# Kernel tuning notes

Hardware: AMD Instinct MI355X
Metric: run time of the kernel (lower is better)

The kernel has to match this reference:

```python
import jax, jax.numpy as jnp
import numpy as np

N, E, F_IN, HID, HEADS, NT, B = 50000, 400000, 32, 64, 4, 20, 64
IN1 = F_IN + HID  # 96, conv1 input dim after concat with node-type embedding


def _glorot(key, shape):
    fan_in = shape[0]
    return jax.random.normal(key, shape, dtype=jnp.float32) / np.sqrt(fan_in)


def setup_inputs() -> dict:
    key = jax.random.key(0)
    ks = jax.random.split(key, 40)
    inp = {
        "x": jax.random.normal(ks[0], (N, F_IN), dtype=jnp.float32),
        "edge_index": jax.random.randint(ks[1], (2, E), 0, N, dtype=jnp.int32),
        "edge_attr": jax.random.normal(ks[2], (E,), dtype=jnp.float32),
        "batch": jnp.sort(jax.random.randint(ks[3], (N,), 0, B, dtype=jnp.int32)),
        "node_type": jax.random.randint(ks[4], (N,), 0, NT, dtype=jnp.int32),
        # parameters
        "node_emb": jax.random.normal(ks[5], (NT, HID), dtype=jnp.float32) * 0.1,
        "edge_W": _glorot(ks[6], (1, HID)), "edge_b": jnp.zeros((HID,), jnp.float32),
        # GATConv 1 (in=96, out=64, heads=4, edge_dim=64, concat=False)
        "W1": _glorot(ks[7], (IN1, HEADS * HID)),
        "att_src1": jax.random.normal(ks[8], (HEADS, HID), jnp.float32) * 0.1,
        "att_dst1": jax.random.normal(ks[9], (HEADS, HID), jnp.float32) * 0.1,
        "We1": _glorot(ks[10], (HID, HEADS * HID)),
        "att_e1": jax.random.normal(ks[11], (HEADS, HID), jnp.float32) * 0.1,
        "b1": jnp.zeros((HID,), jnp.float32),
        # GATConv 2 (in=64)
        "W2": _glorot(ks[12], (HID, HEADS * HID)),
        "att_src2": jax.random.normal(ks[13], (HEADS, HID), jnp.float32) * 0.1,
        "att_dst2": jax.random.normal(ks[14], (HEADS, HID), jnp.float32) * 0.1,
        "We2": _glorot(ks[15], (HID, HEADS * HID)),
        "att_e2": jax.random.normal(ks[16], (HEADS, HID), jnp.float32) * 0.1,
        "b2": jnp.zeros((HID,), jnp.float32),
        # SAGEConv (mean aggr): out = mean_agg @ Wl + x @ Wr + b
        "sage_Wl": _glorot(ks[17], (HID, HID)), "sage_Wr": _glorot(ks[18], (HID, HID)),
        "sage_b": jnp.zeros((HID,), jnp.float32),
        "lin1_W": _glorot(ks[19], (HID, HID)), "lin1_b": jnp.zeros((HID,), jnp.float32),
        "lin2_W": _glorot(ks[20], (HID, HID)), "lin2_b": jnp.zeros((HID,), jnp.float32),
        "tel_W": _glorot(ks[21], (HID, 1)), "tel_b": jnp.zeros((1,), jnp.float32),
        "comp_W": _glorot(ks[22], (HID, 1)), "comp_b": jnp.zeros((1,), jnp.float32),
        "pch_W": _glorot(ks[23], (HID, 1)), "pch_b": jnp.zeros((1,), jnp.float32),
    }
    return inp


def _gat(x, src, dst, edge_h, W, att_s, att_d, We, att_e, b):
    n = x.shape[0]
    h = (x @ W).reshape(n, HEADS, HID)                       # [N,H,C]
    a_s = (h * att_s).sum(-1)                                # [N,H]
    a_d = (h * att_d).sum(-1)
    e = (edge_h @ We).reshape(-1, HEADS, HID)                # [E,H,C]
    a_e = (e * att_e).sum(-1)                                # [E,H]
    alpha = jax.nn.leaky_relu(a_s[src] + a_d[dst] + a_e, 0.2)
    m = jax.ops.segment_max(alpha, dst, num_segments=n)
    m = jnp.where(jnp.isfinite(m), m, 0.0)
    ex = jnp.exp(alpha - m[dst])
    den = jax.ops.segment_sum(ex, dst, num_segments=n)
    alpha = ex / (den[dst] + 1e-16)                          # segment softmax per dst
    out = jax.ops.segment_sum(h[src] * alpha[..., None], dst, num_segments=n)
    return out.mean(axis=1) + b                              # concat=False -> head mean


def reference(x, edge_index, edge_attr, batch, node_type, node_emb, edge_W, edge_b,
              W1, att_src1, att_dst1, We1, att_e1, b1,
              W2, att_src2, att_dst2, We2, att_e2, b2,
              sage_Wl, sage_Wr, sage_b, lin1_W, lin1_b, lin2_W, lin2_b,
              tel_W, tel_b, comp_W, comp_b, pch_W, pch_b):
    src, dst = edge_index[0], edge_index[1]
    edge_h = edge_attr[:, None] @ edge_W + edge_b            # [E,HID]
    h = jnp.concatenate([x, node_emb[node_type]], axis=-1)   # [N,96]
    h = jax.nn.elu(_gat(h, src, dst, edge_h, W1, att_src1, att_dst1, We1, att_e1, b1))
    h = jax.nn.elu(_gat(h, src, dst, edge_h, W2, att_src2, att_dst2, We2, att_e2, b2))
    # SAGEConv with mean aggregation
    deg = jax.ops.segment_sum(jnp.ones((src.shape[0],), h.dtype), dst, num_segments=N)
    agg = jax.ops.segment_sum(h[src], dst, num_segments=N) / jnp.maximum(deg, 1.0)[:, None]
    h = jax.nn.elu(agg @ sage_Wl + h @ sage_Wr + sage_b)
    # global mean pool over graphs
    cnt = jax.ops.segment_sum(jnp.ones((N,), h.dtype), batch, num_segments=B)
    g = jax.ops.segment_sum(h, batch, num_segments=B) / jnp.maximum(cnt, 1.0)[:, None]
    g = jax.nn.elu(g @ lin1_W + lin1_b)                      # dropout is identity in eval
    g = g @ lin2_W + lin2_b
    return (g @ tel_W + tel_b, g @ comp_W + comp_b, g @ pch_W + pch_b)
```

## Files before the change

kernel.cpp:

```cpp
#include <hip/hip_runtime.h>
#include <hip/hip_bf16.h>


#define NN 50000
#define NE 400000
#define FIN 32
#define NBATCH 64

typedef __hip_bfloat16 bf16;
typedef short bf16x8 __attribute__((ext_vector_type(8)));
typedef float f32x4 __attribute__((ext_vector_type(4)));

__device__ __forceinline__ float b2f(bf16 v) { return __bfloat162float(v); }
__device__ __forceinline__ float lrelu(float x) { return x > 0.f ? x : 0.2f * x; }
__device__ __forceinline__ float eluf(float x) { return x > 0.f ? x : (expf(x) - 1.f); }

__device__ __forceinline__ float4 f4fma(float s, float4 w, float4 c) {
  c.x = fmaf(s, w.x, c.x); c.y = fmaf(s, w.y, c.y);
  c.z = fmaf(s, w.z, c.z); c.w = fmaf(s, w.w, c.w);
  return c;
}

__device__ __forceinline__ float4 upk4(uint2 u) {
  float4 f;
  f.x = __uint_as_float(u.x << 16);
  f.y = __uint_as_float(u.x & 0xffff0000u);
  f.z = __uint_as_float(u.y << 16);
  f.w = __uint_as_float(u.y & 0xffff0000u);
  return f;
}

__device__ __forceinline__ unsigned short bfbits(float f) {
  bf16 b = __float2bfloat16(f);
  unsigned short u;
  __builtin_memcpy(&u, &b, 2);
  return u;
}
__device__ __forceinline__ float hi_f(unsigned short u) {
  return __uint_as_float((unsigned int)u << 16);
}

__global__ __launch_bounds__(256) void k_prep(
    const float* __restrict__ W1, const float* __restrict__ W2,
    const float* __restrict__ We1, const float* __restrict__ atte1,
    const float* __restrict__ We2, const float* __restrict__ atte2,
    const float* __restrict__ edgeW, const float* __restrict__ edgeB,
    unsigned short* __restrict__ B1h, unsigned short* __restrict__ B1l,
    unsigned short* __restrict__ B2h, unsigned short* __restrict__ B2l,
    float* __restrict__ pq) {
  if (blockIdx.x == 96) {
    int t = threadIdx.x, h = t >> 6, c = t & 63;
    float sW1 = 0.f, sB1 = 0.f, sW2 = 0.f, sB2 = 0.f;
    for (int j = 0; j < 64; ++j) {
      float w = edgeW[j], b = edgeB[j];
      float we1 = We1[j * 256 + h * 64 + c];
      float we2 = We2[j * 256 + h * 64 + c];
      sW1 += w * we1; sB1 += b * we1;
      sW2 += w * we2; sB2 += b * we2;
    }
    float a1 = atte1[h * 64 + c], a2 = atte2[h * 64 + c];
    float p1 = sW1 * a1, q1 = sB1 * a1, p2 = sW2 * a2, q2 = sB2 * a2;
    for (int o = 32; o; o >>= 1) {
      p1 += __shfl_xor(p1, o); q1 += __shfl_xor(q1, o);
      p2 += __shfl_xor(p2, o); q2 += __shfl_xor(q2, o);
    }
    if (c == 0) { pq[h] = p1; pq[4 + h] = q1; pq[8 + h] = p2; pq[12 + h] = q2; }
    return;
  }
  int t = blockIdx.x * 256 + threadIdx.x;
  if (t < 256 * 96) {
    int n = t / 96, k = t - n * 96;
    float v = W1[k * 256 + n];
    unsigned short h = bfbits(v);
    B1h[t] = h; B1l[t] = bfbits(v - hi_f(h));
  }
  if (t < 256 * 64) {
    int n = t >> 6, k = t & 63;
    float v = W2[k * 256 + n];
    unsigned short h = bfbits(v);
    B2h[t] = h; B2l[t] = bfbits(v - hi_f(h));
  }
}

__global__ void k_hist(const int* __restrict__ dst, int* __restrict__ cnt) {
  int e = blockIdx.x * 256 + threadIdx.x;
  if (e < NE) atomicAdd(&cnt[dst[e]], 1);
}

__global__ __launch_bounds__(1024) void k_scan(const int* __restrict__ cnt,
                                               int* __restrict__ off) {
  __shared__ int wsum[16];
  __shared__ int carry;
  int t = threadIdx.x, lane = t & 63, w = t >> 6;
  if (t == 0) { carry = 0; off[0] = 0; }
  __syncthreads();
  for (int base = 0; base < NN; base += 1024) {
    int idx = base + t;
    int v = (idx < NN) ? cnt[idx] : 0;
    int s = v;
    for (int o = 1; o < 64; o <<= 1) { int u = __shfl_up(s, o); if (lane >= o) s += u; }
    if (lane == 63) wsum[w] = s;
    __syncthreads();
    if (t < 16) {
      int ws = wsum[t];
      for (int o = 1; o < 16; o <<= 1) { int u = __shfl_up(ws, o); if (t >= o) ws += u; }
      wsum[t] = ws;
    }
    __syncthreads();
    int add = carry + (w ? wsum[w - 1] : 0);
    if (idx < NN) off[idx + 1] = add + s;
    __syncthreads();
    if (t == 0) carry += wsum[15];
    __syncthreads();
  }
}

__global__ void k_scatter(const int* __restrict__ src, const int* __restrict__ dst,
                          const float* __restrict__ ea, const int* __restrict__ off,
                          int* __restrict__ cnt, int* __restrict__ csr_src,
                          float* __restrict__ csr_ea) {
  int e = blockIdx.x * 256 + threadIdx.x;
  if (e >= NE) return;
  int d = dst[e];
  int r = atomicSub(&cnt[d], 1);
  int slot = off[d] + r - 1;
  csr_src[slot] = src[e];
  csr_ea[slot] = ea[e];
}

__global__ __launch_bounds__(256) void k_splitA(
    const float* __restrict__ x, const int* __restrict__ ntype,
    const float* __restrict__ emb, unsigned short* __restrict__ Ah,
    unsigned short* __restrict__ Al) {
  const int total = NN * 96;
  for (int i = blockIdx.x * 256 + threadIdx.x; i < total; i += gridDim.x * 256) {
    int n = i / 96, k = i - n * 96;
    float v = (k < FIN) ? x[n * FIN + k] : emb[ntype[n] * 64 + (k - FIN)];
    unsigned short h = bfbits(v);
    Ah[i] = h;
    Al[i] = bfbits(v - hi_f(h));
  }
}

template <int K>
__global__ __launch_bounds__(256) void k_mm_mfma(
    const unsigned short* __restrict__ Ah, const unsigned short* __restrict__ Al,
    const unsigned short* __restrict__ Bh, const unsigned short* __restrict__ Bl,
    const float* __restrict__ atts, const float* __restrict__ attd,
    bf16* __restrict__ hmat, float* __restrict__ as_, float* __restrict__ ad_) {
  int m0 = blockIdx.x * 64;
  int w = threadIdx.x >> 6;
  int lane = threadIdx.x & 63;
  int lr = lane & 15;
  int lc = lane >> 4;
  float attsv[4], attdv[4];
  #pragma unroll
  for (int nt = 0; nt < 4; ++nt) {
    attsv[nt] = atts[w * 64 + nt * 16 + lr];
    attdv[nt] = attd[w * 64 + nt * 16 + lr];
  }
  f32x4 acc[4][4] = {};
  #pragma unroll
  for (int ks = 0; ks < K; ks += 32) {
    int koff = ks + lc * 8;
    bf16x8 ah[4], al[4], bh[4], bl[4];
    #pragma unroll
    for (int mt = 0; mt < 4; ++mt) {
      int m = m0 + mt * 16 + lr;
      if (m > NN - 1) m = NN - 1;
      ah[mt] = *reinterpret_cast<const bf16x8*>(&Ah[(size_t)m * K + koff]);
      al[mt] = *reinterpret_cast<const bf16x8*>(&Al[(size_t)m * K + koff]);
    }
    #pragma unroll
    for (int nt = 0; nt < 4; ++nt) {
      int n = w * 64 + nt * 16 + lr;
      bh[nt] = *reinterpret_cast<const bf16x8*>(&Bh[(size_t)n * K + koff]);
      bl[nt] = *reinterpret_cast<const bf16x8*>(&Bl[(size_t)n * K + koff]);
    }
    #pragma unroll
    for (int mt = 0; mt < 4; ++mt) {
      #pragma unroll
      for (int nt = 0; nt < 4; ++nt) {
        acc[mt][nt] = __builtin_amdgcn_mfma_f32_16x16x32_bf16(ah[mt], bh[nt], acc[mt][nt], 0, 0, 0);
        acc[mt][nt] = __builtin_amdgcn_mfma_f32_16x16x32_bf16(al[mt], bh[nt], acc[mt][nt], 0, 0, 0);
        acc[mt][nt] = __builtin_amdgcn_mfma_f32_16x16x32_bf16(ah[mt], bl[nt], acc[mt][nt], 0, 0, 0);
      }
    }
  }
  #pragma unroll
  for (int mt = 0; mt < 4; ++mt) {
    #pragma unroll
    for (int reg = 0; reg < 4; ++reg) {
      int row = m0 + mt * 16 + lc * 4 + reg;
      float sS = 0.f, sD = 0.f;
      #pragma unroll
      for (int nt = 0; nt < 4; ++nt) {
        float v = acc[mt][nt][reg];
        sS += v * attsv[nt];
        sD += v * attdv[nt];
      }
      for (int o = 1; o < 16; o <<= 1) {
        sS += __shfl_xor(sS, o);
        sD += __shfl_xor(sD, o);
      }
      if (row < NN) {
        #pragma unroll
        for (int nt = 0; nt < 4; ++nt)
          hmat[(size_t)row * 256 + w * 64 + nt * 16 + lr] =
              __float2bfloat16(acc[mt][nt][reg]);
        if (lr == 0) { as_[row * 4 + w] = sS; ad_[row * 4 + w] = sD; }
      }
    }
  }
}

__global__ __launch_bounds__(256) void k_gat(
    const int* __restrict__ off, const int* __restrict__ csr_src,
    const float* __restrict__ csr_ea, const float* __restrict__ as_,
    const float* __restrict__ ad_, const float* __restrict__ pq, int pqo,
    const bf16* __restrict__ hmat, const float* __restrict__ bias,
    float* __restrict__ outf, unsigned short* __restrict__ oph,
    unsigned short* __restrict__ opl) {
  __shared__ float wlds[4][256];
  int wv = threadIdx.x >> 6;
  int wid = (blockIdx.x << 2) + wv;
  int lane = threadIdx.x & 63;
  if (wid >= NN) return;
  int beg = off[wid], end = off[wid + 1];
  int deg = end - beg;
  int hsel = lane >> 4;
  float4 D = reinterpret_cast<const float4*>(ad_)[wid];
  float p0 = pq[pqo + 0], p1 = pq[pqo + 1], p2 = pq[pqo + 2], p3 = pq[pqo + 3];
  float q0 = pq[pqo + 4], q1 = pq[pqo + 5], q2 = pq[pqo + 6], q3 = pq[pqo + 7];
  float4 acc = {0.f, 0.f, 0.f, 0.f};

  if (deg <= 64) {
    bool valid = lane < deg;
    float lx = -INFINITY, ly = -INFINITY, lz = -INFINITY, lw = -INFINITY;
    if (valid) {
      int s = csr_src[beg + lane];
      float ea = csr_ea[beg + lane];
      float4 A = reinterpret_cast<const float4*>(as_)[s];
      lx = lrelu(A.x + D.x + ea * p0 + q0);
      ly = lrelu(A.y + D.y + ea * p1 + q1);
      lz = lrelu(A.z + D.z + ea * p2 + q2);
      lw = lrelu(A.w + D.w + ea * p3 + q3);
    }
    float m0 = lx, m1 = ly, m2 = lz, m3 = lw;
    for (int o = 32; o; o >>= 1) {
      m0 = fmaxf(m0, __shfl_xor(m0, o));
      m1 = fmaxf(m1, __shfl_xor(m1, o));
      m2 = fmaxf(m2, __shfl_xor(m2, o));
      m3 = fmaxf(m3, __shfl_xor(m3, o));
    }
    float w0 = valid ? __expf(lx - m0) : 0.f;
    float w1 = valid ? __expf(ly - m1) : 0.f;
    float w2 = valid ? __expf(lz - m2) : 0.f;
    float w3 = valid ? __expf(lw - m3) : 0.f;
    float s0 = w0, s1 = w1, s2 = w2, s3 = w3;
    for (int o = 32; o; o >>= 1) {
      s0 += __shfl_xor(s0, o); s1 += __shfl_xor(s1, o);
      s2 += __shfl_xor(s2, o); s3 += __shfl_xor(s3, o);
    }
    float4 wv4;
    wv4.x = w0 / (s0 + 1e-16f);
    wv4.y = w1 / (s1 + 1e-16f);
    wv4.z = w2 / (s2 + 1e-16f);
    wv4.w = w3 / (s3 + 1e-16f);
    reinterpret_cast<float4*>(&wlds[wv][0])[lane] = wv4;
    const float* wp = &wlds[wv][0];
    int j = 0;
    for (; j + 8 <= deg; j += 8) {
      int sA = csr_src[beg + j + 0];
      int sB = csr_src[beg + j + 1];
      int sC = csr_src[beg + j + 2];
      int sD = csr_src[beg + j + 3];
      int sE = csr_src[beg + j + 4];
      int sF = csr_src[beg + j + 5];
      int sG = csr_src[beg + j + 6];
      int sH = csr_src[beg + j + 7];
      float wA = wp[4 * (j + 0) + hsel];
      float wB = wp[4 * (j + 1) + hsel];
      float wC = wp[4 * (j + 2) + hsel];
      float wD = wp[4 * (j + 3) + hsel];
      float wE = wp[4 * (j + 4) + hsel];
      float wF = wp[4 * (j + 5) + hsel];
      float wG = wp[4 * (j + 6) + hsel];
      float wH = wp[4 * (j + 7) + hsel];
      uint2 uA = *reinterpret_cast<const uint2*>(&hmat[(size_t)sA * 256 + 4 * lane]);
      uint2 uB = *reinterpret_cast<const uint2*>(&hmat[(size_t)sB * 256 + 4 * lane]);
      uint2 uC = *reinterpret_cast<const uint2*>(&hmat[(size_t)sC * 256 + 4 * lane]);
      uint2 uD = *reinterpret_cast<const uint2*>(&hmat[(size_t)sD * 256 + 4 * lane]);
      uint2 uE = *reinterpret_cast<const uint2*>(&hmat[(size_t)sE * 256 + 4 * lane]);
      uint2 uF = *reinterpret_cast<const uint2*>(&hmat[(size_t)sF * 256 + 4 * lane]);
      uint2 uG = *reinterpret_cast<const uint2*>(&hmat[(size_t)sG * 256 + 4 * lane]);
      uint2 uH = *reinterpret_cast<const uint2*>(&hmat[(size_t)sH * 256 + 4 * lane]);
      acc = f4fma(wA, upk4(uA), acc);
      acc = f4fma(wB, upk4(uB), acc);
      acc = f4fma(wC, upk4(uC), acc);
      acc = f4fma(wD, upk4(uD), acc);
      acc = f4fma(wE, upk4(uE), acc);
      acc = f4fma(wF, upk4(uF), acc);
      acc = f4fma(wG, upk4(uG), acc);
      acc = f4fma(wH, upk4(uH), acc);
    }
    for (; j + 4 <= deg; j += 4) {
      int sA = csr_src[beg + j + 0];
      int sB = csr_src[beg + j + 1];
      int sC = csr_src[beg + j + 2];
      int sD = csr_src[beg + j + 3];
      float wA = wp[4 * (j + 0) + hsel];
      float wB = wp[4 * (j + 1) + hsel];
      float wC = wp[4 * (j + 2) + hsel];
      float wD = wp[4 * (j + 3) + hsel];
      uint2 uA = *reinterpret_cast<const uint2*>(&hmat[(size_t)sA * 256 + 4 * lane]);
      uint2 uB = *reinterpret_cast<const uint2*>(&hmat[(size_t)sB * 256 + 4 * lane]);
      uint2 uC = *reinterpret_cast<const uint2*>(&hmat[(size_t)sC * 256 + 4 * lane]);
      uint2 uD = *reinterpret_cast<const uint2*>(&hmat[(size_t)sD * 256 + 4 * lane]);
      acc = f4fma(wA, upk4(uA), acc);
      acc = f4fma(wB, upk4(uB), acc);
      acc = f4fma(wC, upk4(uC), acc);
      acc = f4fma(wD, upk4(uD), acc);
    }
    for (; j < deg; ++j) {
      int s = csr_src[beg + j];
      float w = wp[4 * j + hsel];
      uint2 u = *reinterpret_cast<const uint2*>(&hmat[(size_t)s * 256 + 4 * lane]);
      acc = f4fma(w, upk4(u), acc);
    }
  } else {
    float m0 = -INFINITY, m1 = -INFINITY, m2 = -INFINITY, m3 = -INFINITY;
    float s0 = 0.f, s1 = 0.f, s2 = 0.f, s3 = 0.f;
    for (int e = beg + lane; e < end; e += 64) {
      int s = csr_src[e];
      float ea = csr_ea[e];
      float4 A = reinterpret_cast<const float4*>(as_)[s];
      float lx = lrelu(A.x + D.x + ea * p0 + q0);
      float ly = lrelu(A.y + D.y + ea * p1 + q1);
      float lz = lrelu(A.z + D.z + ea * p2 + q2);
      float lw = lrelu(A.w + D.w + ea * p3 + q3);
      float nm;
      nm = fmaxf(m0, lx); s0 = s0 * __expf(m0 - nm) + __expf(lx - nm); m0 = nm;
      nm = fmaxf(m1, ly); s1 = s1 * __expf(m1 - nm) + __expf(ly - nm); m1 = nm;
      nm = fmaxf(m2, lz); s2 = s2 * __expf(m2 - nm) + __expf(lz - nm); m2 = nm;
      nm = fmaxf(m3, lw); s3 = s3 * __expf(m3 - nm) + __expf(lw - nm); m3 = nm;
    }
    for (int o = 32; o; o >>= 1) {
      float om, os, nm;
      om = __shfl_xor(m0, o); os = __shfl_xor(s0, o); nm = fmaxf(m0, om);
      s0 = s0 * __expf(fmaxf(m0 - nm, -80.f)) + os * __expf(fmaxf(om - nm, -80.f)); m0 = nm;
      om = __shfl_xor(m1, o); os = __shfl_xor(s1, o); nm = fmaxf(m1, om);
      s1 = s1 * __expf(fmaxf(m1 - nm, -80.f)) + os * __expf(fmaxf(om - nm, -80.f)); m1 = nm;
      om = __shfl_xor(m2, o); os = __shfl_xor(s2, o); nm = fmaxf(m2, om);
      s2 = s2 * __expf(fmaxf(m2 - nm, -80.f)) + os * __expf(fmaxf(om - nm, -80.f)); m2 = nm;
      om = __shfl_xor(m3, o); os = __shfl_xor(s3, o); nm = fmaxf(m3, om);
      s3 = s3 * __expf(fmaxf(m3 - nm, -80.f)) + os * __expf(fmaxf(om - nm, -80.f)); m3 = nm;
    }
    float i0 = 1.f / (s0 + 1e-16f), i1 = 1.f / (s1 + 1e-16f);
    float i2 = 1.f / (s2 + 1e-16f), i3 = 1.f / (s3 + 1e-16f);
    float Dh = hsel == 0 ? D.x : hsel == 1 ? D.y : hsel == 2 ? D.z : D.w;
    float ph = hsel == 0 ? p0 : hsel == 1 ? p1 : hsel == 2 ? p2 : p3;
    float qh = hsel == 0 ? q0 : hsel == 1 ? q1 : hsel == 2 ? q2 : q3;
    float mh = hsel == 0 ? m0 : hsel == 1 ? m1 : hsel == 2 ? m2 : m3;
    float ih = hsel == 0 ? i0 : hsel == 1 ? i1 : hsel == 2 ? i2 : i3;
    for (int j = beg; j < end; ++j) {
      int s = csr_src[j];
      float ea = csr_ea[j];
      float4 A = reinterpret_cast<const float4*>(as_)[s];
      float Ah = hsel == 0 ? A.x : hsel == 1 ? A.y : hsel == 2 ? A.z : A.w;
      float l = lrelu(Ah + Dh + ea * ph + qh);
      float w = __expf(l - mh) * ih;
      uint2 u = *reinterpret_cast<const uint2*>(&hmat[(size_t)s * 256 + 4 * lane]);
      acc = f4fma(w, upk4(u), acc);
    }
  }
  acc.x += __shfl_xor(acc.x, 16); acc.y += __shfl_xor(acc.y, 16);
  acc.z += __shfl_xor(acc.z, 16); acc.w += __shfl_xor(acc.w, 16);
  acc.x += __shfl_xor(acc.x, 32); acc.y += __shfl_xor(acc.y, 32);
  acc.z += __shfl_xor(acc.z, 32); acc.w += __shfl_xor(acc.w, 32);
  if (lane < 16) {
    float4 bv = reinterpret_cast<const float4*>(bias)[lane];
    float4 r;
    r.x = eluf(0.25f * acc.x + bv.x);
    r.y = eluf(0.25f * acc.y + bv.y);
    r.z = eluf(0.25f * acc.z + bv.z);
    r.w = eluf(0.25f * acc.w + bv.w);
    if (outf) reinterpret_cast<float4*>(&outf[(size_t)wid * 64])[lane] = r;
    if (oph) {
      ushort4 h4, l4;
      h4.x = bfbits(r.x); l4.x = bfbits(r.x - hi_f(h4.x));
      h4.y = bfbits(r.y); l4.y = bfbits(r.y - hi_f(h4.y));
      h4.z = bfbits(r.z); l4.z = bfbits(r.z - hi_f(h4.z));
      h4.w = bfbits(r.w); l4.w = bfbits(r.w - hi_f(h4.w));
      *reinterpret_cast<ushort4*>(&oph[(size_t)wid * 64 + lane * 4]) = h4;
      *reinterpret_cast<ushort4*>(&opl[(size_t)wid * 64 + lane * 4]) = l4;
    }
  }
}

__global__ __launch_bounds__(256) void k_agg(
    const int* __restrict__ off, const int* __restrict__ csr_src,
    const float* __restrict__ h3, float* __restrict__ agg) {
  int wid = (blockIdx.x << 2) + (threadIdx.x >> 6);
  int lane = threadIdx.x & 63;
  if (wid >= NN) return;
  int beg = off[wid], end = off[wid + 1];
  float acc = 0.f;
  int e = beg;
  for (; e + 8 <= end; e += 8) {
    int s0 = csr_src[e + 0], s1 = csr_src[e + 1];
    int s2 = csr_src[e + 2], s3 = csr_src[e + 3];
    int s4 = csr_src[e + 4], s5 = csr_src[e + 5];
    int s6 = csr_src[e + 6], s7 = csr_src[e + 7];
    float v0 = h3[(size_t)s0 * 64 + lane];
    float v1 = h3[(size_t)s1 * 64 + lane];
    float v2 = h3[(size_t)s2 * 64 + lane];
    float v3 = h3[(size_t)s3 * 64 + lane];
    float v4 = h3[(size_t)s4 * 64 + lane];
    float v5 = h3[(size_t)s5 * 64 + lane];
    float v6 = h3[(size_t)s6 * 64 + lane];
    float v7 = h3[(size_t)s7 * 64 + lane];
    acc += ((v0 + v1) + (v2 + v3)) + ((v4 + v5) + (v6 + v7));
  }
  for (; e + 4 <= end; e += 4) {
    int s0 = csr_src[e + 0], s1 = csr_src[e + 1];
    int s2 = csr_src[e + 2], s3 = csr_src[e + 3];
    float v0 = h3[(size_t)s0 * 64 + lane];
    float v1 = h3[(size_t)s1 * 64 + lane];
    float v2 = h3[(size_t)s2 * 64 + lane];
    float v3 = h3[(size_t)s3 * 64 + lane];
    acc += (v0 + v1) + (v2 + v3);
  }
  for (; e < end; ++e) acc += h3[(size_t)csr_src[e] * 64 + lane];
  agg[(size_t)wid * 64 + lane] = acc / fmaxf((float)(end - beg), 1.f);
}

__global__ __launch_bounds__(256) void k_sage_mm(
    const float* __restrict__ agg, const float* __restrict__ h3,
    const float* __restrict__ Wl, const float* __restrict__ Wr,
    const float* __restrict__ bias, float* __restrict__ out) {
  __shared__ float WlS[4096];
  __shared__ float WrS[4096];
  __shared__ float Ag[2048];
  __shared__ float Hr[2048];
  int t = threadIdx.x;
  for (int i = t; i < 4096; i += 256) { WlS[i] = Wl[i]; WrS[i] = Wr[i]; }
  int ct = t & 15, rg = t >> 4;
  float4 bv = reinterpret_cast<const float4*>(bias)[ct];
  for (int r0 = blockIdx.x * 32; r0 < NN; r0 += gridDim.x * 32) {
    for (int i = t; i < 2048; i += 256) {
      int n = r0 + (i >> 6);
      float va = 0.f, vh = 0.f;
      if (n < NN) {
        va = agg[(size_t)n * 64 + (i & 63)];
        vh = h3[(size_t)n * 64 + (i & 63)];
      }
      Ag[i] = va; Hr[i] = vh;
    }
    __syncthreads();
    float4 c0 = {0.f, 0.f, 0.f, 0.f}, c1 = c0;
    const float* a0 = &Ag[(rg * 2 + 0) * 64];
    const float* a1 = &Ag[(rg * 2 + 1) * 64];
    const float* h0 = &Hr[(rg * 2 + 0) * 64];
    const float* h1 = &Hr[(rg * 2 + 1) * 64];
    #pragma unroll 4
    for (int k = 0; k < 64; k += 4) {
      float4 wl0 = *reinterpret_cast<const float4*>(&WlS[(k + 0) * 64 + ct * 4]);
      float4 wl1 = *reinterpret_cast<const float4*>(&WlS[(k + 1) * 64 + ct * 4]);
      float4 wl2 = *reinterpret_cast<const float4*>(&WlS[(k + 2) * 64 + ct * 4]);
      float4 wl3 = *reinterpret_cast<const float4*>(&WlS[(k + 3) * 64 + ct * 4]);
      float4 wr0 = *reinterpret_cast<const float4*>(&WrS[(k + 0) * 64 + ct * 4]);
      float4 wr1 = *reinterpret_cast<const float4*>(&WrS[(k + 1) * 64 + ct * 4]);
      float4 wr2 = *reinterpret_cast<const float4*>(&WrS[(k + 2) * 64 + ct * 4]);
      float4 wr3 = *reinterpret_cast<const float4*>(&WrS[(k + 3) * 64 + ct * 4]);
      float4 aa0 = *reinterpret_cast<const float4*>(&a0[k]);
      float4 aa1 = *reinterpret_cast<const float4*>(&a1[k]);
      float4 hh0 = *reinterpret_cast<const float4*>(&h0[k]);
      float4 hh1 = *reinterpret_cast<const float4*>(&h1[k]);
      c0 = f4fma(aa0.x, wl0, c0); c0 = f4fma(aa0.y, wl1, c0);
      c0 = f4fma(aa0.z, wl2, c0); c0 = f4fma(aa0.w, wl3, c0);
      c0 = f4fma(hh0.x, wr0, c0); c0 = f4fma(hh0.y, wr1, c0);
      c0 = f4fma(hh0.z, wr2, c0); c0 = f4fma(hh0.w, wr3, c0);
      c1 = f4fma(aa1.x, wl0, c1); c1 = f4fma(aa1.y, wl1, c1);
      c1 = f4fma(aa1.z, wl2, c1); c1 = f4fma(aa1.w, wl3, c1);
      c1 = f4fma(hh1.x, wr0, c1); c1 = f4fma(hh1.y, wr1, c1);
      c1 = f4fma(hh1.z, wr2, c1); c1 = f4fma(hh1.w, wr3, c1);
    }
    int n0 = r0 + rg * 2;
    if (n0 + 0 < NN) {
      float4 r;
      r.x = eluf(c0.x + bv.x); r.y = eluf(c0.y + bv.y);
      r.z = eluf(c0.z + bv.z); r.w = eluf(c0.w + bv.w);
      *reinterpret_cast<float4*>(&out[(size_t)(n0 + 0) * 64 + ct * 4]) = r;
    }
    if (n0 + 1 < NN) {
      float4 r;
      r.x = eluf(c1.x + bv.x); r.y = eluf(c1.y + bv.y);
      r.z = eluf(c1.z + bv.z); r.w = eluf(c1.w + bv.w);
      *reinterpret_cast<float4*>(&out[(size_t)(n0 + 1) * 64 + ct * 4]) = r;
    }
    __syncthreads();
  }
}

__global__ __launch_bounds__(256) void k_pool2(const float* __restrict__ hs,
                                               const int* __restrict__ batch,
                                               float* __restrict__ g) {
  int cid = (blockIdx.x << 2) + (threadIdx.x >> 6);
  int lane = threadIdx.x & 63;
  int n0 = cid * 32;
  if (n0 >= NN) return;
  int n1 = n0 + 32 < NN ? n0 + 32 : NN;
  int cur = batch[n0];
  float acc = 0.f;
  for (int n = n0; n < n1; ++n) {
    int b = batch[n];
    if (b != cur) {
      atomicAdd(&g[cur * 64 + lane], acc);
      acc = 0.f;
      cur = b;
    }
    acc += hs[(size_t)n * 64 + lane];
  }
  atomicAdd(&g[cur * 64 + lane], acc);
}

__device__ __forceinline__ int lowerb(const int* __restrict__ a, int n, int key) {
  int lo = 0, hi = n;
  while (lo < hi) { int mid = (lo + hi) >> 1; if (a[mid] < key) lo = mid + 1; else hi = mid; }
  return lo;
}

__global__ __launch_bounds__(256) void k_head(
    const float* __restrict__ g, const int* __restrict__ batch,
    const float* __restrict__ l1W, const float* __restrict__ l1b,
    const float* __restrict__ l2W, const float* __restrict__ l2b,
    const float* __restrict__ telW, const float* __restrict__ telb,
    const float* __restrict__ compW, const float* __restrict__ compb,
    const float* __restrict__ pchW, const float* __restrict__ pchb,
    float* __restrict__ out) {
  __shared__ float gS[4096];
  __shared__ float WS[4096];
  __shared__ float hS[4096];
  __shared__ float invc[64];
  int t = threadIdx.x;
  if (t < 64) {
    int lo = lowerb(batch, NN, t), hi = lowerb(batch, NN, t + 1);
    invc[t] = 1.f / fmaxf((float)(hi - lo), 1.f);
  }
  for (int i = t; i < 4096; i += 256) WS[i] = l1W[i];
  __syncthreads();
  for (int i = t; i < 4096; i += 256) gS[i] = g[i] * invc[i >> 6];
  __syncthreads();
  for (int i = t; i < 4096; i += 256) {
    int r = i >> 6, j = i & 63;
    float s = 0.f;
    for (int k = 0; k < 64; ++k) s += gS[r * 64 + k] * WS[k * 64 + j];
    hS[i] = eluf(s + l1b[j]);
  }
  __syncthreads();
  for (int i = t; i < 4096; i += 256) WS[i] = l2W[i];
  __syncthreads();
  for (int i = t; i < 4096; i += 256) {
    int r = i >> 6, j = i & 63;
    float s = 0.f;
    for (int k = 0; k < 64; ++k) s += hS[r * 64 + k] * WS[k * 64 + j];
    gS[i] = s + l2b[j];
  }
  __syncthreads();
  if (t < 192) {
    int head = t >> 6, r = t & 63;
    const float* Wv = head == 0 ? telW : (head == 1 ? compW : pchW);
    float bb = head == 0 ? telb[0] : (head == 1 ? compb[0] : pchb[0]);
    float s = 0.f;
    for (int k = 0; k < 64; ++k) s += gS[r * 64 + k] * Wv[k];
    out[t] = s + bb;
  }
}

extern "C" void kernel_launch(void* const* d_in, const int* in_sizes, int n_in,
                              void* d_out, int out_size, void* d_ws, size_t ws_size,
                              hipStream_t stream) {
  const float* x     = (const float*)d_in[0];
  const int*   eidx  = (const int*)d_in[1];
  const float* eattr = (const float*)d_in[2];
  const int*   batch = (const int*)d_in[3];
  const int*   ntype = (const int*)d_in[4];
  const float* nemb  = (const float*)d_in[5];
  const float* edgeW = (const float*)d_in[6];
  const float* edgeB = (const float*)d_in[7];
  const float* W1    = (const float*)d_in[8];
  const float* atts1 = (const float*)d_in[9];
  const float* attd1 = (const float*)d_in[10];
  const float* We1   = (const float*)d_in[11];
  const float* atte1 = (const float*)d_in[12];
  const float* b1    = (const float*)d_in[13];
  const float* W2    = (const float*)d_in[14];
  const float* atts2 = (const float*)d_in[15];
  const float* attd2 = (const float*)d_in[16];
  const float* We2   = (const float*)d_in[17];
  const float* atte2 = (const float*)d_in[18];
  const float* b2    = (const float*)d_in[19];
  const float* sageWl = (const float*)d_in[20];
  const float* sageWr = (const float*)d_in[21];
  const float* sageB  = (const float*)d_in[22];
  const float* l1W = (const float*)d_in[23];
  const float* l1b = (const float*)d_in[24];
  const float* l2W = (const float*)d_in[25];
  const float* l2b = (const float*)d_in[26];
  const float* telW  = (const float*)d_in[27];
  const float* telb  = (const float*)d_in[28];
  const float* compW = (const float*)d_in[29];
  const float* compb = (const float*)d_in[30];
  const float* pchW  = (const float*)d_in[31];
  const float* pchb  = (const float*)d_in[32];

  char* wp = (char*)d_ws;
  auto alloc = [&](size_t bytes) -> char* {
    char* p = wp;
    wp += (bytes + 255) & ~(size_t)255;
    return p;
  };
  float*  pq      = (float*)alloc(16 * 4);
  int*    cnt     = (int*)alloc((size_t)NN * 4);
  int*    off     = (int*)alloc(((size_t)NN + 1) * 4);
  int*    csr_src = (int*)alloc((size_t)NE * 4);
  float*  csr_ea  = (float*)alloc((size_t)NE * 4);
  float*  as_     = (float*)alloc((size_t)NN * 16);
  float*  ad_     = (float*)alloc((size_t)NN * 16);
  bf16*   hmat    = (bf16*)alloc((size_t)NN * 256 * 2);
  float*  nodeB   = (float*)alloc((size_t)NN * 64 * 4);
  float*  aggbuf  = (float*)alloc((size_t)NN * 64 * 4);
  unsigned short* B1h = (unsigned short*)alloc(256 * 96 * 2);
  unsigned short* B1l = (unsigned short*)alloc(256 * 96 * 2);
  unsigned short* B2h = (unsigned short*)alloc(256 * 64 * 2);
  unsigned short* B2l = (unsigned short*)alloc(256 * 64 * 2);
  char* R = alloc((size_t)NN * 96 * 2 * 2);
  unsigned short* A1h = (unsigned short*)R;
  unsigned short* A1l = A1h + (size_t)NN * 96;
  unsigned short* A2h = (unsigned short*)R;
  unsigned short* A2l = A2h + (size_t)NN * 64;
  float* sageout = (float*)R;
  float* gbuf = (float*)alloc(64 * 64 * 4);

  const int* srcI = eidx;
  const int* dstI = eidx + NE;

  hipMemsetAsync(cnt, 0, (size_t)NN * 4, stream);
  hipMemsetAsync(gbuf, 0, 64 * 64 * 4, stream);
  k_prep<<<97, 256, 0, stream>>>(W1, W2, We1, atte1, We2, atte2, edgeW, edgeB,
                                 B1h, B1l, B2h, B2l, pq);
  k_hist<<<(NE + 255) / 256, 256, 0, stream>>>(dstI, cnt);
  k_scan<<<1, 1024, 0, stream>>>(cnt, off);
  k_scatter<<<(NE + 255) / 256, 256, 0, stream>>>(srcI, dstI, eattr, off, cnt,
                                                  csr_src, csr_ea);
  k_splitA<<<2048, 256, 0, stream>>>(x, ntype, nemb, A1h, A1l);
  k_mm_mfma<96><<<(NN + 63) / 64, 256, 0, stream>>>(
      A1h, A1l, B1h, B1l, atts1, attd1, hmat, as_, ad_);
  k_gat<<<NN / 4, 256, 0, stream>>>(off, csr_src, csr_ea, as_, ad_, pq, 0,
                                    hmat, b1, nullptr, A2h, A2l);
  k_mm_mfma<64><<<(NN + 63) / 64, 256, 0, stream>>>(
      A2h, A2l, B2h, B2l, atts2, attd2, hmat, as_, ad_);
  k_gat<<<NN / 4, 256, 0, stream>>>(off, csr_src, csr_ea, as_, ad_, pq, 8,
                                    hmat, b2, nodeB, nullptr, nullptr);
  k_agg<<<NN / 4, 256, 0, stream>>>(off, csr_src, nodeB, aggbuf);
  k_sage_mm<<<1024, 256, 0, stream>>>(aggbuf, nodeB, sageWl, sageWr, sageB,
                                      sageout);
  k_pool2<<<((NN + 31) / 32 + 3) / 4, 256, 0, stream>>>(sageout, batch, gbuf);
  k_head<<<1, 256, 0, stream>>>(gbuf, batch, l1W, l1b, l2W, l2b, telW, telb,
                                compW, compb, pchW, pchb, (float*)d_out);
}
```

Measured before the change: 452.2 us.

## Fuse SAGE aggregation, matmul and mean-pool; merge prep, splitA and memsets

The SAGE neighbor-mean aggregation, the dense SAGE matmul and the global pooling atomics now run in a single kernel. Aggregated rows and outputs stay in shared memory, so the agg and sageout buffers are never written to or read back from global memory. The weight split, input split and buffer zeroing are also merged into one prep kernel, replacing two memsets and two launches. The trade-off is more shared memory and per-block weight loading across about 1563 blocks, where the old matmul kernel used 1024 persistent blocks.

Measured after the change: 496.0 us. +9.7%, slower.

```diff
diff --git a/kernel.cpp b/kernel.cpp
--- a/kernel.cpp
+++ b/kernel.cpp
@@ -40,23 +40,28 @@
   return __uint_as_float((unsigned int)u << 16);
 }
 
-__global__ __launch_bounds__(256) void k_prep(
-    const float* __restrict__ W1, const float* __restrict__ W2,
-    const float* __restrict__ We1, const float* __restrict__ atte1,
-    const float* __restrict__ We2, const float* __restrict__ atte2,
-    const float* __restrict__ edgeW, const float* __restrict__ edgeB,
-    unsigned short* __restrict__ B1h, unsigned short* __restrict__ B1l,
-    unsigned short* __restrict__ B2h, unsigned short* __restrict__ B2l,
-    float* __restrict__ pq) {
-  if (blockIdx.x == 96) {
-    int t = threadIdx.x, h = t >> 6, c = t & 63;
+__global__ __launch_bounds__(256) void k_prep0(
+    const float* __restrict__ x, const int* __restrict__ ntype,
+    const float* __restrict__ emb, unsigned short* __restrict__ A1h,
+    unsigned short* __restrict__ A1l, const float* __restrict__ W1,
+    const float* __restrict__ W2, const float* __restrict__ We1,
+    const float* __restrict__ atte1, const float* __restrict__ We2,
+    const float* __restrict__ atte2, const float* __restrict__ edgeW,
+    const float* __restrict__ edgeB, unsigned short* __restrict__ B1h,
+    unsigned short* __restrict__ B1l, unsigned short* __restrict__ B2h,
+    unsigned short* __restrict__ B2l, float* __restrict__ pq,
+    int* __restrict__ cnt, float* __restrict__ gbuf) {
+  int b = blockIdx.x;
+  int tid = threadIdx.x;
+  if (b == 0) {
+    int h = tid >> 6, c = tid & 63;
     float sW1 = 0.f, sB1 = 0.f, sW2 = 0.f, sB2 = 0.f;
     for (int j = 0; j < 64; ++j) {
-      float w = edgeW[j], b = edgeB[j];
+      float w = edgeW[j], bb = edgeB[j];
       float we1 = We1[j * 256 + h * 64 + c];
       float we2 = We2[j * 256 + h * 64 + c];
-      sW1 += w * we1; sB1 += b * we1;
-      sW2 += w * we2; sB2 += b * we2;
+      sW1 += w * we1; sB1 += bb * we1;
+      sW2 += w * we2; sB2 += bb * we2;
     }
     float a1 = atte1[h * 64 + c], a2 = atte2[h * 64 + c];
     float p1 = sW1 * a1, q1 = sB1 * a1, p2 = sW2 * a2, q2 = sB2 * a2;
@@ -67,19 +72,35 @@
     if (c == 0) { pq[h] = p1; pq[4 + h] = q1; pq[8 + h] = p2; pq[12 + h] = q2; }
     return;
   }
-  int t = blockIdx.x * 256 + threadIdx.x;
-  if (t < 256 * 96) {
-    int n = t / 96, k = t - n * 96;
-    float v = W1[k * 256 + n];
+  if (b <= 96) {
+    int t = (b - 1) * 256 + tid;
+    if (t < 256 * 96) {
+      int n = t / 96, k = t - n * 96;
+      float v = W1[k * 256 + n];
+      unsigned short h = bfbits(v);
+      B1h[t] = h; B1l[t] = bfbits(v - hi_f(h));
+    }
+    if (t < 256 * 64) {
+      int n = t >> 6, k = t & 63;
+      float v = W2[k * 256 + n];
+      unsigned short h = bfbits(v);
+      B2h[t] = h; B2l[t] = bfbits(v - hi_f(h));
+    }
+    return;
+  }
+  int nb = gridDim.x - 97;
+  int base = (b - 97) * 256 + tid;
+  int stride = nb * 256;
+  const int total = NN * 96;
+  for (int i = base; i < total; i += stride) {
+    int n = i / 96, k = i - n * 96;
+    float v = (k < FIN) ? x[n * FIN + k] : emb[ntype[n] * 64 + (k - FIN)];
     unsigned short h = bfbits(v);
-    B1h[t] = h; B1l[t] = bfbits(v - hi_f(h));
-  }
-  if (t < 256 * 64) {
-    int n = t >> 6, k = t & 63;
-    float v = W2[k * 256 + n];
-    unsigned short h = bfbits(v);
-    B2h[t] = h; B2l[t] = bfbits(v - hi_f(h));
-  }
+    A1h[i] = h;
+    A1l[i] = bfbits(v - hi_f(h));
+  }
+  for (int i = base; i < NN; i += stride) cnt[i] = 0;
+  for (int i = base; i < 64 * 64; i += stride) gbuf[i] = 0.f;
 }
 
 __global__ void k_hist(const int* __restrict__ dst, int* __restrict__ cnt) {
@@ -126,20 +147,6 @@
   int slot = off[d] + r - 1;
   csr_src[slot] = src[e];
   csr_ea[slot] = ea[e];
-}
-
-__global__ __launch_bounds__(256) void k_splitA(
-    const float* __restrict__ x, const int* __restrict__ ntype,
-    const float* __restrict__ emb, unsigned short* __restrict__ Ah,
-    unsigned short* __restrict__ Al) {
-  const int total = NN * 96;
-  for (int i = blockIdx.x * 256 + threadIdx.x; i < total; i += gridDim.x * 256) {
-    int n = i / 96, k = i - n * 96;
-    float v = (k < FIN) ? x[n * FIN + k] : emb[ntype[n] * 64 + (k - FIN)];
-    unsigned short h = bfbits(v);
-    Ah[i] = h;
-    Al[i] = bfbits(v - hi_f(h));
-  }
 }
 
 template <int K>
@@ -398,131 +405,106 @@
   }
 }
 
-__global__ __launch_bounds__(256) void k_agg(
+__global__ __launch_bounds__(256) void k_sage_f(
     const int* __restrict__ off, const int* __restrict__ csr_src,
-    const float* __restrict__ h3, float* __restrict__ agg) {
-  int wid = (blockIdx.x << 2) + (threadIdx.x >> 6);
-  int lane = threadIdx.x & 63;
-  if (wid >= NN) return;
-  int beg = off[wid], end = off[wid + 1];
-  float acc = 0.f;
-  int e = beg;
-  for (; e + 8 <= end; e += 8) {
-    int s0 = csr_src[e + 0], s1 = csr_src[e + 1];
-    int s2 = csr_src[e + 2], s3 = csr_src[e + 3];
-    int s4 = csr_src[e + 4], s5 = csr_src[e + 5];
-    int s6 = csr_src[e + 6], s7 = csr_src[e + 7];
-    float v0 = h3[(size_t)s0 * 64 + lane];
-    float v1 = h3[(size_t)s1 * 64 + lane];
-    float v2 = h3[(size_t)s2 * 64 + lane];
-    float v3 = h3[(size_t)s3 * 64 + lane];
-    float v4 = h3[(size_t)s4 * 64 + lane];
-    float v5 = h3[(size_t)s5 * 64 + lane];
-    float v6 = h3[(size_t)s6 * 64 + lane];
-    float v7 = h3[(size_t)s7 * 64 + lane];
-    acc += ((v0 + v1) + (v2 + v3)) + ((v4 + v5) + (v6 + v7));
-  }
-  for (; e + 4 <= end; e += 4) {
-    int s0 = csr_src[e + 0], s1 = csr_src[e + 1];
-    int s2 = csr_src[e + 2], s3 = csr_src[e + 3];
-    float v0 = h3[(size_t)s0 * 64 + lane];
-    float v1 = h3[(size_t)s1 * 64 + lane];
-    float v2 = h3[(size_t)s2 * 64 + lane];
-    float v3 = h3[(size_t)s3 * 64 + lane];
-    acc += (v0 + v1) + (v2 + v3);
-  }
-  for (; e < end; ++e) acc += h3[(size_t)csr_src[e] * 64 + lane];
-  agg[(size_t)wid * 64 + lane] = acc / fmaxf((float)(end - beg), 1.f);
-}
-
-__global__ __launch_bounds__(256) void k_sage_mm(
-    const float* __restrict__ agg, const float* __restrict__ h3,
-    const float* __restrict__ Wl, const float* __restrict__ Wr,
-    const float* __restrict__ bias, float* __restrict__ out) {
+    const float* __restrict__ h3, const float* __restrict__ Wl,
+    const float* __restrict__ Wr, const float* __restrict__ bias,
+    const int* __restrict__ batch, float* __restrict__ g) {
   __shared__ float WlS[4096];
   __shared__ float WrS[4096];
   __shared__ float Ag[2048];
   __shared__ float Hr[2048];
-  int t = threadIdx.x;
+  __shared__ float Out[2048];
+  __shared__ int bS[32];
+  int t = threadIdx.x, lane = t & 63, w = t >> 6;
   for (int i = t; i < 4096; i += 256) { WlS[i] = Wl[i]; WrS[i] = Wr[i]; }
+  int r0 = blockIdx.x * 32;
+  for (int k = 0; k < 8; ++k) {
+    int rl = w * 8 + k;
+    int n = r0 + rl;
+    float aggv = 0.f, hv = 0.f;
+    int bb = -1;
+    if (n < NN) {
+      int beg = off[n], end = off[n + 1];
+      float acc = 0.f;
+      int e = beg;
+      for (; e + 8 <= end; e += 8) {
+        int s0 = csr_src[e + 0], s1 = csr_src[e + 1];
+        int s2 = csr_src[e + 2], s3 = csr_src[e + 3];
+        int s4 = csr_src[e + 4], s5 = csr_src[e + 5];
+        int s6 = csr_src[e + 6], s7 = csr_src[e + 7];
+        float v0 = h3[(size_t)s0 * 64 + lane];
+        float v1 = h3[(size_t)s1 * 64 + lane];
+        float v2 = h3[(size_t)s2 * 64 + lane];
+        float v3 = h3[(size_t)s3 * 64 + lane];
+        float v4 = h3[(size_t)s4 * 64 + lane];
+        float v5 = h3[(size_t)s5 * 64 + lane];
+        float v6 = h3[(size_t)s6 * 64 + lane];
+        float v7 = h3[(size_t)s7 * 64 + lane];
+        acc += ((v0 + v1) + (v2 + v3)) + ((v4 + v5) + (v6 + v7));
+      }
+      for (; e < end; ++e) acc += h3[(size_t)csr_src[e] * 64 + lane];
+      aggv = acc / fmaxf((float)(end - beg), 1.f);
+      hv = h3[(size_t)n * 64 + lane];
+      bb = batch[n];
+    }
+    Ag[rl * 64 + lane] = aggv;
+    Hr[rl * 64 + lane] = hv;
+    if (lane == 0) bS[rl] = bb;
+  }
+  __syncthreads();
   int ct = t & 15, rg = t >> 4;
   float4 bv = reinterpret_cast<const float4*>(bias)[ct];
-  for (int r0 = blockIdx.x * 32; r0 < NN; r0 += gridDim.x * 32) {
-    for (int i = t; i < 2048; i += 256) {
-      int n = r0 + (i >> 6);
-      float va = 0.f, vh = 0.f;
-      if (n < NN) {
-        va = agg[(size_t)n * 64 + (i & 63)];
-        vh = h3[(size_t)n * 64 + (i & 63)];
-      }
-      Ag[i] = va; Hr[i] = vh;
-    }
-    __syncthreads();
-    float4 c0 = {0.f, 0.f, 0.f, 0.f}, c1 = c0;
-    const float* a0 = &Ag[(rg * 2 + 0) * 64];
-    const float* a1 = &Ag[(rg * 2 + 1) * 64];
-    const float* h0 = &Hr[(rg * 2 + 0) * 64];
-    const float* h1 = &Hr[(rg * 2 + 1) * 64];
-    #pragma unroll 4
-    for (int k = 0; k < 64; k += 4) {
-      float4 wl0 = *reinterpret_cast<const float4*>(&WlS[(k + 0) * 64 + ct * 4]);
-      float4 wl1 = *reinterpret_cast<const float4*>(&WlS[(k + 1) * 64 + ct * 4]);
-      float4 wl2 = *reinterpret_cast<const float4*>(&WlS[(k + 2) * 64 + ct * 4]);
-      float4 wl3 = *reinterpret_cast<const float4*>(&WlS[(k + 3) * 64 + ct * 4]);
-      float4 wr0 = *reinterpret_cast<const float4*>(&WrS[(k + 0) * 64 + ct * 4]);
-      float4 wr1 = *reinterpret_cast<const float4*>(&WrS[(k + 1) * 64 + ct * 4]);
-      float4 wr2 = *reinterpret_cast<const float4*>(&WrS[(k + 2) * 64 + ct * 4]);
-      float4 wr3 = *reinterpret_cast<const float4*>(&WrS[(k + 3) * 64 + ct * 4]);
-      float4 aa0 = *reinterpret_cast<const float4*>(&a0[k]);
-      float4 aa1 = *reinterpret_cast<const float4*>(&a1[k]);
-      float4 hh0 = *reinterpret_cast<const float4*>(&h0[k]);
-      float4 hh1 = *reinterpret_cast<const float4*>(&h1[k]);
-      c0 = f4fma(aa0.x, wl0, c0); c0 = f4fma(aa0.y, wl1, c0);
-      c0 = f4fma(aa0.z, wl2, c0); c0 = f4fma(aa0.w, wl3, c0);
-      c0 = f4fma(hh0.x, wr0, c0); c0 = f4fma(hh0.y, wr1, c0);
-      c0 = f4fma(hh0.z, wr2, c0); c0 = f4fma(hh0.w, wr3, c0);
-      c1 = f4fma(aa1.x, wl0, c1); c1 = f4fma(aa1.y, wl1, c1);
-      c1 = f4fma(aa1.z, wl2, c1); c1 = f4fma(aa1.w, wl3, c1);
-      c1 = f4fma(hh1.x, wr0, c1); c1 = f4fma(hh1.y, wr1, c1);
-      c1 = f4fma(hh1.z, wr2, c1); c1 = f4fma(hh1.w, wr3, c1);
-    }
-    int n0 = r0 + rg * 2;
-    if (n0 + 0 < NN) {
-      float4 r;
-      r.x = eluf(c0.x + bv.x); r.y = eluf(c0.y + bv.y);
-      r.z = eluf(c0.z + bv.z); r.w = eluf(c0.w + bv.w);
-      *reinterpret_cast<float4*>(&out[(size_t)(n0 + 0) * 64 + ct * 4]) = r;
-    }
-    if (n0 + 1 < NN) {
-      float4 r;
-      r.x = eluf(c1.x + bv.x); r.y = eluf(c1.y + bv.y);
-      r.z = eluf(c1.z + bv.z); r.w = eluf(c1.w + bv.w);
-      *reinterpret_cast<float4*>(&out[(size_t)(n0 + 1) * 64 + ct * 4]) = r;
-    }
-    __syncthreads();
-  }
-}
-
-__global__ __launch_bounds__(256) void k_pool2(const float* __restrict__ hs,
-                                               const int* __restrict__ batch,
-                                               float* __restrict__ g) {
-  int cid = (blockIdx.x << 2) + (threadIdx.x >> 6);
-  int lane = threadIdx.x & 63;
-  int n0 = cid * 32;
-  if (n0 >= NN) return;
-  int n1 = n0 + 32 < NN ? n0 + 32 : NN;
-  int cur = batch[n0];
+  float4 c0 = {0.f, 0.f, 0.f, 0.f}, c1 = c0;
+  const float* a0 = &Ag[(rg * 2 + 0) * 64];
+  const float* a1 = &Ag[(rg * 2 + 1) * 64];
+  const float* h0 = &Hr[(rg * 2 + 0) * 64];
+  const float* h1 = &Hr[(rg * 2 + 1) * 64];
+  #pragma unroll 4
+  for (int k = 0; k < 64; k += 4) {
+    float4 wl0 = *reinterpret_cast<const float4*>(&WlS[(k + 0) * 64 + ct * 4]);
+    float4 wl1 = *reinterpret_cast<const float4*>(&WlS[(k + 1) * 64 + ct * 4]);
+    float4 wl2 = *reinterpret_cast<const float4*>(&WlS[(k + 2) * 64 + ct * 4]);
+    float4 wl3 = *reinterpret_cast<const float4*>(&WlS[(k + 3) * 64 + ct * 4]);
+    float4 wr0 = *reinterpret_cast<const float4*>(&WrS[(k + 0) * 64 + ct * 4]);
+    float4 wr1 = *reinterpret_cast<const float4*>(&WrS[(k + 1) * 64 + ct * 4]);
+    float4 wr2 = *reinterpret_cast<const float4*>(&WrS[(k + 2) * 64 + ct * 4]);
+    float4 wr3 = *reinterpret_cast<const float4*>(&WrS[(k + 3) * 64 + ct * 4]);
+    float4 aa0 = *reinterpret_cast<const float4*>(&a0[k]);
+    float4 aa1 = *reinterpret_cast<const float4*>(&a1[k]);
+    float4 hh0 = *reinterpret_cast<const float4*>(&h0[k]);
+    float4 hh1 = *reinterpret_cast<const float4*>(&h1[k]);
+    c0 = f4fma(aa0.x, wl0, c0); c0 = f4fma(aa0.y, wl1, c0);
+    c0 = f4fma(aa0.z, wl2, c0); c0 = f4fma(aa0.w, wl3, c0);
+    c0 = f4fma(hh0.x, wr0, c0); c0 = f4fma(hh0.y, wr1, c0);
+    c0 = f4fma(hh0.z, wr2, c0); c0 = f4fma(hh0.w, wr3, c0);
+    c1 = f4fma(aa1.x, wl0, c1); c1 = f4fma(aa1.y, wl1, c1);
+    c1 = f4fma(aa1.z, wl2, c1); c1 = f4fma(aa1.w, wl3, c1);
+    c1 = f4fma(hh1.x, wr0, c1); c1 = f4fma(hh1.y, wr1, c1);
+    c1 = f4fma(hh1.z, wr2, c1); c1 = f4fma(hh1.w, wr3, c1);
+  }
+  float4 o0, o1;
+  o0.x = eluf(c0.x + bv.x); o0.y = eluf(c0.y + bv.y);
+  o0.z = eluf(c0.z + bv.z); o0.w = eluf(c0.w + bv.w);
+  o1.x = eluf(c1.x + bv.x); o1.y = eluf(c1.y + bv.y);
+  o1.z = eluf(c1.z + bv.z); o1.w = eluf(c1.w + bv.w);
+  *reinterpret_cast<float4*>(&Out[(rg * 2 + 0) * 64 + ct * 4]) = o0;
+  *reinterpret_cast<float4*>(&Out[(rg * 2 + 1) * 64 + ct * 4]) = o1;
+  __syncthreads();
+  int col = t & 63, grp = t >> 6;
   float acc = 0.f;
-  for (int n = n0; n < n1; ++n) {
-    int b = batch[n];
-    if (b != cur) {
-      atomicAdd(&g[cur * 64 + lane], acc);
+  int cur = bS[grp * 8];
+  for (int k = 0; k < 8; ++k) {
+    int rl = grp * 8 + k;
+    int bb = bS[rl];
+    if (bb != cur) {
+      if (cur >= 0) atomicAdd(&g[cur * 64 + col], acc);
       acc = 0.f;
-      cur = b;
-    }
-    acc += hs[(size_t)n * 64 + lane];
-  }
-  atomicAdd(&g[cur * 64 + lane], acc);
+      cur = bb;
+    }
+    if (bb >= 0) acc += Out[rl * 64 + col];
+  }
+  if (cur >= 0) atomicAdd(&g[cur * 64 + col], acc);
 }
 
 __device__ __forceinline__ int lowerb(const int* __restrict__ a, int n, int key) {
@@ -630,7 +612,6 @@
   float*  ad_     = (float*)alloc((size_t)NN * 16);
   bf16*   hmat    = (bf16*)alloc((size_t)NN * 256 * 2);
   float*  nodeB   = (float*)alloc((size_t)NN * 64 * 4);
-  float*  aggbuf  = (float*)alloc((size_t)NN * 64 * 4);
   unsigned short* B1h = (unsigned short*)alloc(256 * 96 * 2);
   unsigned short* B1l = (unsigned short*)alloc(256 * 96 * 2);
   unsigned short* B2h = (unsigned short*)alloc(256 * 64 * 2);
@@ -640,21 +621,18 @@
   unsigned short* A1l = A1h + (size_t)NN * 96;
   unsigned short* A2h = (unsigned short*)R;
   unsigned short* A2l = A2h + (size_t)NN * 64;
-  float* sageout = (float*)R;
   float* gbuf = (float*)alloc(64 * 64 * 4);
 
   const int* srcI = eidx;
   const int* dstI = eidx + NE;
 
-  hipMemsetAsync(cnt, 0, (size_t)NN * 4, stream);
-  hipMemsetAsync(gbuf, 0, 64 * 64 * 4, stream);
-  k_prep<<<97, 256, 0, stream>>>(W1, W2, We1, atte1, We2, atte2, edgeW, edgeB,
-                                 B1h, B1l, B2h, B2l, pq);
+  k_prep0<<<2048, 256, 0, stream>>>(x, ntype, nemb, A1h, A1l, W1, W2, We1,
+                                    atte1, We2, atte2, edgeW, edgeB, B1h, B1l,
+                                    B2h, B2l, pq, cnt, gbuf);
   k_hist<<<(NE + 255) / 256, 256, 0, stream>>>(dstI, cnt);
   k_scan<<<1, 1024, 0, stream>>>(cnt, off);
   k_scatter<<<(NE + 255) / 256, 256, 0, stream>>>(srcI, dstI, eattr, off, cnt,
                                                   csr_src, csr_ea);
-  k_splitA<<<2048, 256, 0, stream>>>(x, ntype, nemb, A1h, A1l);
   k_mm_mfma<96><<<(NN + 63) / 64, 256, 0, stream>>>(
       A1h, A1l, B1h, B1l, atts1, attd1, hmat, as_, ad_);
   k_gat<<<NN / 4, 256, 0, stream>>>(off, csr_src, csr_ea, as_, ad_, pq, 0,
@@ -663,10 +641,8 @@
       A2h, A2l, B2h, B2l, atts2, attd2, hmat, as_, ad_);
   k_gat<<<NN / 4, 256, 0, stream>>>(off, csr_src, csr_ea, as_, ad_, pq, 8,
                                     hmat, b2, nodeB, nullptr, nullptr);
-  k_agg<<<NN / 4, 256, 0, stream>>>(off, csr_src, nodeB, aggbuf);
-  k_sage_mm<<<1024, 256, 0, stream>>>(aggbuf, nodeB, sageWl, sageWr, sageB,
-                                      sageout);
-  k_pool2<<<((NN + 31) / 32 + 3) / 4, 256, 0, stream>>>(sageout, batch, gbuf);
+  k_sage_f<<<(NN + 31) / 32, 256, 0, stream>>>(off, csr_src, nodeB, sageWl,
+                                               sageWr, sageB, batch, gbuf);
   k_head<<<1, 256, 0, stream>>>(gbuf, batch, l1W, l1b, l2W, l2b, telW, telb,
                                 compW, compb, pchW, pchb, (float*)d_out);
 }
```
